# Optimization experiments

Hardware: AMD Instinct MI355X
Metric: run time of the kernel (lower is better)

The kernel has to match this reference:

```python
import jax, jax.numpy as jnp
import numpy as np

H = 64  # hidden_size hardcoded in the module


def _lstm_scan(x_pre, w_hh):
    # x_pre: [T, B, 4H] = x @ W_ih^T + b_ih + b_hh, precomputed for all steps
    # w_hh: [4H, H]. PyTorch gate order: i, f, g, o.
    B = x_pre.shape[1]
    h0 = jnp.zeros((B, H), x_pre.dtype)
    c0 = jnp.zeros((B, H), x_pre.dtype)

    def cell(carry, xp):
        h, c = carry
        gates = xp + h @ w_hh.T  # [B, 4H]
        i, f, g, o = jnp.split(gates, 4, axis=-1)
        i = jax.nn.sigmoid(i)
        f = jax.nn.sigmoid(f)
        g = jnp.tanh(g)
        o = jax.nn.sigmoid(o)
        c = f * c + i * g
        h = o * jnp.tanh(c)
        return (h, c), h

    _, hs = jax.lax.scan(cell, (h0, c0), x_pre)
    return hs  # [T, B, H]


def _bidir_layer(x, w_ih, w_hh, b_ih, b_hh):
    # x: [T, B, D]; w_ih: [2, 4H, D]; w_hh: [2, 4H, H]; b_*: [2, 4H]
    pre_f = jnp.einsum('tbd,gd->tbg', x, w_ih[0]) + b_ih[0] + b_hh[0]
    hs_f = _lstm_scan(pre_f, w_hh[0])
    xr = x[::-1]
    pre_b = jnp.einsum('tbd,gd->tbg', xr, w_ih[1]) + b_ih[1] + b_hh[1]
    hs_b = _lstm_scan(pre_b, w_hh[1])[::-1]  # re-reverse to align with time
    return jnp.concatenate([hs_f, hs_b], axis=-1)  # [T, B, 2H]


def setup_inputs() -> dict:
    key = jax.random.key(0)
    B, T, F = 1024, 512, 32
    ks = jax.random.split(key, 11)
    s = 1.0 / float(np.sqrt(H))  # PyTorch LSTM init: U(-1/sqrt(H), 1/sqrt(H))
    u = lambda k, shape: jax.random.uniform(k, shape, jnp.float32, -s, s)
    return dict(
        x=jax.random.normal(ks[0], (B, T, F), jnp.float32),
        w_ih0=u(ks[1], (2, 4 * H, F)),
        w_hh0=u(ks[2], (2, 4 * H, H)),
        b_ih0=u(ks[3], (2, 4 * H)),
        b_hh0=u(ks[4], (2, 4 * H)),
        w_ih1=u(ks[5], (2, 4 * H, 2 * H)),
        w_hh1=u(ks[6], (2, 4 * H, H)),
        b_ih1=u(ks[7], (2, 4 * H)),
        b_hh1=u(ks[8], (2, 4 * H)),
        fc_w=u(ks[9], (2, 2 * H)),
        fc_b=u(ks[10], (2,)),
    )


def reference(x, w_ih0, w_hh0, b_ih0, b_hh0, w_ih1, w_hh1, b_ih1, b_hh1, fc_w, fc_b):
    xt = jnp.transpose(x, (1, 0, 2))  # [T, B, F]
    h1 = _bidir_layer(xt, w_ih0, w_hh0, b_ih0, b_hh0)  # [T, B, 2H]
    h2 = _bidir_layer(h1, w_ih1, w_hh1, b_ih1, b_hh1)  # [T, B, 2H]
    last = h2[-1]  # out[:, -1, :] in batch_first layout -> [B, 2H]
    return last @ fc_w.T + fc_b  # [B, 2]
```

## Files before the change

kernel.cpp:

```cpp
#include <hip/hip_runtime.h>

#define TT 512
#define BB 1024
#define FF 32
#define HH 64
#define GG 256

__device__ float g_h1[(size_t)TT * BB * 2 * HH];
__device__ float g_pre0[(size_t)2 * TT * BB * GG];
__device__ float g_pre1[(size_t)TT * BB * GG];
__device__ float g_hf[(size_t)BB * HH];

__device__ __forceinline__ float fsigm(float x) {
    float e = __builtin_amdgcn_exp2f(x * -1.44269504088896f);
    return __builtin_amdgcn_rcpf(1.0f + e);
}
__device__ __forceinline__ float ftanh(float x) {
    float e = __builtin_amdgcn_exp2f(x * -2.88539008177793f);
    return 2.0f * __builtin_amdgcn_rcpf(1.0f + e) - 1.0f;
}
__device__ __forceinline__ float rlane(float v, int l) {
    return __int_as_float(__builtin_amdgcn_readlane(__float_as_int(v), l));
}

__global__ __launch_bounds__(256, 4) void pre_gemm0(
    const float* __restrict__ x,
    const float* __restrict__ w_ih,
    const float* __restrict__ b_ih,
    const float* __restrict__ b_hh)
{
    const int tid = threadIdx.x;
    const int b   = blockIdx.x >> 1;
    const int dir = blockIdx.x & 1;

    __shared__ __align__(16) float4 w4[8 * 256];
    __shared__ __align__(16) float xbuf[2][256];

    const float4* wsrc = (const float4*)(w_ih + ((size_t)dir * GG + tid) * FF);
#pragma unroll
    for (int kq = 0; kq < 8; ++kq) w4[kq * 256 + tid] = wsrc[kq];
    const float bias = b_ih[dir * GG + tid] + b_hh[dir * GG + tid];

    const float* xbase = x + (size_t)b * TT * FF;
    xbuf[0][tid] = xbase[tid];
    const size_t OS = (size_t)BB * GG;

    for (int tc = 0; tc < 64; ++tc) {
        const int cur = tc & 1;
        __syncthreads();

        float vnext = 0.f;
        if (tc + 1 < 64) vnext = xbase[(tc + 1) * 256 + tid];

        float a0 = bias, a1 = bias, a2 = bias, a3 = bias,
              a4 = bias, a5 = bias, a6 = bias, a7 = bias;
#pragma unroll
        for (int kq = 0; kq < 8; ++kq) {
            float4 wq = w4[kq * 256 + tid];
            const float4* xr = (const float4*)xbuf[cur];
            float4 q;
            q = xr[0 * 8 + kq]; a0 += q.x*wq.x + q.y*wq.y + q.z*wq.z + q.w*wq.w;
            q = xr[1 * 8 + kq]; a1 += q.x*wq.x + q.y*wq.y + q.z*wq.z + q.w*wq.w;
            q = xr[2 * 8 + kq]; a2 += q.x*wq.x + q.y*wq.y + q.z*wq.z + q.w*wq.w;
            q = xr[3 * 8 + kq]; a3 += q.x*wq.x + q.y*wq.y + q.z*wq.z + q.w*wq.w;
            q = xr[4 * 8 + kq]; a4 += q.x*wq.x + q.y*wq.y + q.z*wq.z + q.w*wq.w;
            q = xr[5 * 8 + kq]; a5 += q.x*wq.x + q.y*wq.y + q.z*wq.z + q.w*wq.w;
            q = xr[6 * 8 + kq]; a6 += q.x*wq.x + q.y*wq.y + q.z*wq.z + q.w*wq.w;
            q = xr[7 * 8 + kq]; a7 += q.x*wq.x + q.y*wq.y + q.z*wq.z + q.w*wq.w;
        }
        float* op = g_pre0 + (((size_t)dir * TT + tc * 8) * BB + b) * GG + tid;
        op[0] = a0; op[1 * OS] = a1; op[2 * OS] = a2; op[3 * OS] = a3;
        op[4 * OS] = a4; op[5 * OS] = a5; op[6 * OS] = a6; op[7 * OS] = a7;

        if (tc + 1 < 64) xbuf[1 - cur][tid] = vnext;
    }
}

#define PINQ(wq) \
    asm volatile("" : "+v"(wq.x), "+v"(wq.y), "+v"(wq.z), "+v"(wq.w))

template <int L>
__global__ __launch_bounds__(64, 1) void lstm_scan(
    const float* __restrict__ w_hh)
{
    const int l   = threadIdx.x;
    const int dir = (L == 0) ? (blockIdx.x & 1) : 0;
    const int b   = (L == 0) ? (int)(blockIdx.x >> 1) : (int)blockIdx.x;

    const float* wbase = w_hh + (size_t)dir * GG * HH;

    const float4* pi_ = (const float4*)(wbase + (size_t)(0  + l) * HH);
    const float4* pf_ = (const float4*)(wbase + (size_t)(64 + l) * HH);
    float4 wi0 = pi_[0],  wi1 = pi_[1],  wi2 = pi_[2],  wi3 = pi_[3],
           wi4 = pi_[4],  wi5 = pi_[5],  wi6 = pi_[6],  wi7 = pi_[7],
           wi8 = pi_[8],  wi9 = pi_[9],  wi10 = pi_[10], wi11 = pi_[11],
           wi12 = pi_[12], wi13 = pi_[13], wi14 = pi_[14], wi15 = pi_[15];
    float4 wf0 = pf_[0],  wf1 = pf_[1],  wf2 = pf_[2],  wf3 = pf_[3],
           wf4 = pf_[4],  wf5 = pf_[5],  wf6 = pf_[6],  wf7 = pf_[7],
           wf8 = pf_[8],  wf9 = pf_[9],  wf10 = pf_[10], wf11 = pf_[11],
           wf12 = pf_[12], wf13 = pf_[13], wf14 = pf_[14], wf15 = pf_[15];
    PINQ(wi0);  PINQ(wi1);  PINQ(wi2);  PINQ(wi3);
    PINQ(wi4);  PINQ(wi5);  PINQ(wi6);  PINQ(wi7);
    PINQ(wi8);  PINQ(wi9);  PINQ(wi10); PINQ(wi11);
    PINQ(wi12); PINQ(wi13); PINQ(wi14); PINQ(wi15);
    PINQ(wf0);  PINQ(wf1);  PINQ(wf2);  PINQ(wf3);
    PINQ(wf4);  PINQ(wf5);  PINQ(wf6);  PINQ(wf7);
    PINQ(wf8);  PINQ(wf9);  PINQ(wf10); PINQ(wf11);
    PINQ(wf12); PINQ(wf13); PINQ(wf14); PINQ(wf15);

    float4 wg[16], wo[16];
    {
        const float4* pg_ = (const float4*)(wbase + (size_t)(128 + l) * HH);
        const float4* po_ = (const float4*)(wbase + (size_t)(192 + l) * HH);
#pragma unroll
        for (int q = 0; q < 16; ++q) { wg[q] = pg_[q]; wo[q] = po_[q]; }
    }

    const float* pre = (L == 0) ? (g_pre0 + (size_t)dir * TT * BB * GG) : g_pre1;

    float c = 0.f, h = 0.f;

    const int t0 = dir ? (TT - 1) : 0;
    const int t1 = dir ? (TT - 2) : 1;
    const float* pp0 = pre + ((size_t)t0 * BB + b) * GG;
    const float* pp1 = pre + ((size_t)t1 * BB + b) * GG;
    float ci0 = pp0[l], cf0 = pp0[64 + l], cg0 = pp0[128 + l], co0 = pp0[192 + l];
    float ci1 = pp1[l], cf1 = pp1[64 + l], cg1 = pp1[128 + l], co1 = pp1[192 + l];

    for (int s = 0; s < TT; ++s) {
        const int t = dir ? (TT - 1 - s) : s;

        float ni = 0.f, nf = 0.f, ng = 0.f, no_ = 0.f;
        if (s + 2 < TT) {
            const int tn = dir ? (TT - 3 - s) : (s + 2);
            const float* np = pre + ((size_t)tn * BB + b) * GG;
            ni = np[l]; nf = np[64 + l]; ng = np[128 + l]; no_ = np[192 + l];
        }

        float ai = ci0, af = cf0, ag = cg0, ao = co0;

#define STEPQ(q) do {                                                        \
        float s0 = rlane(h, 4*q+0), s1 = rlane(h, 4*q+1),                    \
              s2 = rlane(h, 4*q+2), s3 = rlane(h, 4*q+3);                    \
        ai += s0*wi##q.x + s1*wi##q.y + s2*wi##q.z + s3*wi##q.w;             \
        af += s0*wf##q.x + s1*wf##q.y + s2*wf##q.z + s3*wf##q.w;             \
        ag += s0*wg[q].x + s1*wg[q].y + s2*wg[q].z + s3*wg[q].w;             \
        ao += s0*wo[q].x + s1*wo[q].y + s2*wo[q].z + s3*wo[q].w;             \
    } while (0)

        STEPQ(0);  STEPQ(1);  STEPQ(2);  STEPQ(3);
        STEPQ(4);  STEPQ(5);  STEPQ(6);  STEPQ(7);
        STEPQ(8);  STEPQ(9);  STEPQ(10); STEPQ(11);
        STEPQ(12); STEPQ(13); STEPQ(14); STEPQ(15);
#undef STEPQ

        const float ig = fsigm(ai);
        const float fg = fsigm(af);
        const float gg = ftanh(ag);
        const float og = fsigm(ao);
        c = fg * c + ig * gg;
        h = og * ftanh(c);

        if (L == 0) {
            g_h1[((size_t)t * BB + b) * (2 * HH) + dir * HH + l] = h;
        } else {
            if (s == TT - 1) g_hf[(size_t)b * HH + l] = h;
        }

        ci0 = ci1; cf0 = cf1; cg0 = cg1; co0 = co1;
        ci1 = ni;  cf1 = nf;  cg1 = ng;  co1 = no_;
    }
}

#define FMA4(c, s, b) do { c.x += (s)*(b).x; c.y += (s)*(b).y; \
                           c.z += (s)*(b).z; c.w += (s)*(b).w; } while (0)

__global__ __launch_bounds__(256, 2) void pre_gemm1(
    const float* __restrict__ w_ih,
    const float* __restrict__ b_ih,
    const float* __restrict__ b_hh)
{
    __shared__ __align__(16) float As[64 * 132];
    __shared__ __align__(16) float Bs[128 * 68];

    const int tid   = threadIdx.x;
    const int mbase = (int)(blockIdx.x >> 2) * 64;
    const int n0    = (int)(blockIdx.x & 3) * 64;

#pragma unroll
    for (int i = 0; i < 8; ++i) {
        const int qid = tid + 256 * i;
        const int r = qid >> 5, q = qid & 31;
        float4 v = *(const float4*)(g_h1 + (size_t)(mbase + r) * 128 + q * 4);
        *(float4*)(&As[r * 132 + q * 4]) = v;
    }
#pragma unroll
    for (int i = 0; i < 8; ++i) {
        const int qid = tid + 256 * i;
        const int r = qid >> 5, q = qid & 31;
        float4 v = *(const float4*)(w_ih + (size_t)(n0 + r) * 128 + q * 4);
        Bs[(q * 4 + 0) * 68 + r] = v.x;
        Bs[(q * 4 + 1) * 68 + r] = v.y;
        Bs[(q * 4 + 2) * 68 + r] = v.z;
        Bs[(q * 4 + 3) * 68 + r] = v.w;
    }
    __syncthreads();

    const int tx = tid & 15, ty = tid >> 4;

    float4 c0 = make_float4(0.f, 0.f, 0.f, 0.f);
    float4 c1 = c0, c2 = c0, c3 = c0;

#pragma unroll 8
    for (int kq = 0; kq < 32; ++kq) {
        const float4 a0 = *(const float4*)&As[(ty * 4 + 0) * 132 + kq * 4];
        const float4 a1 = *(const float4*)&As[(ty * 4 + 1) * 132 + kq * 4];
        const float4 a2 = *(const float4*)&As[(ty * 4 + 2) * 132 + kq * 4];
        const float4 a3 = *(const float4*)&As[(ty * 4 + 3) * 132 + kq * 4];
        const float4 b0 = *(const float4*)&Bs[(kq * 4 + 0) * 68 + tx * 4];
        const float4 b1 = *(const float4*)&Bs[(kq * 4 + 1) * 68 + tx * 4];
        const float4 b2 = *(const float4*)&Bs[(kq * 4 + 2) * 68 + tx * 4];
        const float4 b3 = *(const float4*)&Bs[(kq * 4 + 3) * 68 + tx * 4];
        FMA4(c0, a0.x, b0); FMA4(c0, a0.y, b1); FMA4(c0, a0.z, b2); FMA4(c0, a0.w, b3);
        FMA4(c1, a1.x, b0); FMA4(c1, a1.y, b1); FMA4(c1, a1.z, b2); FMA4(c1, a1.w, b3);
        FMA4(c2, a2.x, b0); FMA4(c2, a2.y, b1); FMA4(c2, a2.z, b2); FMA4(c2, a2.w, b3);
        FMA4(c3, a3.x, b0); FMA4(c3, a3.y, b1); FMA4(c3, a3.z, b2); FMA4(c3, a3.w, b3);
    }

    float4 bias4;
    bias4.x = b_ih[n0 + tx * 4 + 0] + b_hh[n0 + tx * 4 + 0];
    bias4.y = b_ih[n0 + tx * 4 + 1] + b_hh[n0 + tx * 4 + 1];
    bias4.z = b_ih[n0 + tx * 4 + 2] + b_hh[n0 + tx * 4 + 2];
    bias4.w = b_ih[n0 + tx * 4 + 3] + b_hh[n0 + tx * 4 + 3];

    FMA4(c0, 1.f, bias4); FMA4(c1, 1.f, bias4);
    FMA4(c2, 1.f, bias4); FMA4(c3, 1.f, bias4);

    float* ob = g_pre1 + (size_t)(mbase + ty * 4) * GG + n0 + tx * 4;
    *(float4*)(ob + 0 * (size_t)GG) = c0;
    *(float4*)(ob + 1 * (size_t)GG) = c1;
    *(float4*)(ob + 2 * (size_t)GG) = c2;
    *(float4*)(ob + 3 * (size_t)GG) = c3;
}

#define FMAC4(W, P0, P1, P2, P3, K) do{                                   \
    float4 v_;                                                           \
    v_ = (P0)[K]; acc0 += W.x*v_.x; acc0 += W.y*v_.y; acc0 += W.z*v_.z; acc0 += W.w*v_.w; \
    v_ = (P1)[K]; acc1 += W.x*v_.x; acc1 += W.y*v_.y; acc1 += W.z*v_.z; acc1 += W.w*v_.w; \
    v_ = (P2)[K]; acc2 += W.x*v_.x; acc2 += W.y*v_.y; acc2 += W.z*v_.z; acc2 += W.w*v_.w; \
    v_ = (P3)[K]; acc3 += W.x*v_.x; acc3 += W.y*v_.y; acc3 += W.z*v_.z; acc3 += W.w*v_.w; \
}while(0)

__global__ __launch_bounds__(256, 2) void lstm_final(
    const float* __restrict__ w_ih,
    const float* __restrict__ b_ih,
    const float* __restrict__ b_hh,
    const float* __restrict__ fc_w,
    const float* __restrict__ fc_b,
    float* __restrict__ out)
{
    const int tid = threadIdx.x;
    const int b0  = blockIdx.x * 4;

    __shared__ __align__(16) float x_lds[4][128];
    __shared__ __align__(16) float gact[4][GG];
    __shared__ __align__(16) float last[4][128];

#pragma unroll
    for (int r = 0; r < 2; ++r) {
        int idx = tid + r * 256;
        int b = idx >> 7, col = idx & 127;
        x_lds[b][col] = g_h1[((size_t)(TT - 1) * BB + (b0 + b)) * 128 + col];
    }

    const float4* p = (const float4*)(w_ih + ((size_t)GG + tid) * 128);
    float4 w0 = p[0],  w1 = p[1],  w2 = p[2],  w3 = p[3],  w4 = p[4],  w5 = p[5],
           w6 = p[6],  w7 = p[7],  w8 = p[8],  w9 = p[9],  w10 = p[10], w11 = p[11],
           w12 = p[12], w13 = p[13], w14 = p[14], w15 = p[15], w16 = p[16], w17 = p[17],
           w18 = p[18], w19 = p[19], w20 = p[20], w21 = p[21], w22 = p[22], w23 = p[23],
           w24 = p[24], w25 = p[25], w26 = p[26], w27 = p[27], w28 = p[28], w29 = p[29],
           w30 = p[30], w31 = p[31];
    const float bias = b_ih[GG + tid] + b_hh[GG + tid];
    __syncthreads();

    const float4* xb0 = (const float4*)x_lds[0];
    const float4* xb1 = (const float4*)x_lds[1];
    const float4* xb2 = (const float4*)x_lds[2];
    const float4* xb3 = (const float4*)x_lds[3];

    float acc0 = bias, acc1 = bias, acc2 = bias, acc3 = bias;
    FMAC4(w0, xb0, xb1, xb2, xb3, 0);   FMAC4(w1, xb0, xb1, xb2, xb3, 1);
    FMAC4(w2, xb0, xb1, xb2, xb3, 2);   FMAC4(w3, xb0, xb1, xb2, xb3, 3);
    FMAC4(w4, xb0, xb1, xb2, xb3, 4);   FMAC4(w5, xb0, xb1, xb2, xb3, 5);
    FMAC4(w6, xb0, xb1, xb2, xb3, 6);   FMAC4(w7, xb0, xb1, xb2, xb3, 7);
    FMAC4(w8, xb0, xb1, xb2, xb3, 8);   FMAC4(w9, xb0, xb1, xb2, xb3, 9);
    FMAC4(w10, xb0, xb1, xb2, xb3, 10); FMAC4(w11, xb0, xb1, xb2, xb3, 11);
    FMAC4(w12, xb0, xb1, xb2, xb3, 12); FMAC4(w13, xb0, xb1, xb2, xb3, 13);
    FMAC4(w14, xb0, xb1, xb2, xb3, 14); FMAC4(w15, xb0, xb1, xb2, xb3, 15);
    FMAC4(w16, xb0, xb1, xb2, xb3, 16); FMAC4(w17, xb0, xb1, xb2, xb3, 17);
    FMAC4(w18, xb0, xb1, xb2, xb3, 18); FMAC4(w19, xb0, xb1, xb2, xb3, 19);
    FMAC4(w20, xb0, xb1, xb2, xb3, 20); FMAC4(w21, xb0, xb1, xb2, xb3, 21);
    FMAC4(w22, xb0, xb1, xb2, xb3, 22); FMAC4(w23, xb0, xb1, xb2, xb3, 23);
    FMAC4(w24, xb0, xb1, xb2, xb3, 24); FMAC4(w25, xb0, xb1, xb2, xb3, 25);
    FMAC4(w26, xb0, xb1, xb2, xb3, 26); FMAC4(w27, xb0, xb1, xb2, xb3, 27);
    FMAC4(w28, xb0, xb1, xb2, xb3, 28); FMAC4(w29, xb0, xb1, xb2, xb3, 29);
    FMAC4(w30, xb0, xb1, xb2, xb3, 30); FMAC4(w31, xb0, xb1, xb2, xb3, 31);

    const bool is_g = ((tid >> 6) == 2);
    gact[0][tid] = is_g ? ftanh(acc0) : fsigm(acc0);
    gact[1][tid] = is_g ? ftanh(acc1) : fsigm(acc1);
    gact[2][tid] = is_g ? ftanh(acc2) : fsigm(acc2);
    gact[3][tid] = is_g ? ftanh(acc3) : fsigm(acc3);
    __syncthreads();

    {
        const int cb = tid >> 6, cj = tid & 63;
        float ig = gact[cb][cj];
        float gg = gact[cb][2 * HH + cj];
        float og = gact[cb][3 * HH + cj];
        float c = ig * gg;
        float h = og * ftanh(c);
        last[cb][HH + cj] = h;
        last[cb][cj] = g_hf[(size_t)(b0 + cb) * HH + cj];
    }
    __syncthreads();

    if (tid < 8) {
        int b = tid >> 1, o = tid & 1;
        float a = fc_b[o];
#pragma unroll
        for (int j = 0; j < 128; ++j) a += fc_w[o * 128 + j] * last[b][j];
        out[(size_t)(b0 + b) * 2 + o] = a;
    }
}

extern "C" void kernel_launch(void* const* d_in, const int* in_sizes, int n_in,
                              void* d_out, int out_size, void* d_ws, size_t ws_size,
                              hipStream_t stream) {
    const float* x     = (const float*)d_in[0];
    const float* w_ih0 = (const float*)d_in[1];
    const float* w_hh0 = (const float*)d_in[2];
    const float* b_ih0 = (const float*)d_in[3];
    const float* b_hh0 = (const float*)d_in[4];
    const float* w_ih1 = (const float*)d_in[5];
    const float* w_hh1 = (const float*)d_in[6];
    const float* b_ih1 = (const float*)d_in[7];
    const float* b_hh1 = (const float*)d_in[8];
    const float* fc_w  = (const float*)d_in[9];
    const float* fc_b  = (const float*)d_in[10];
    float* out = (float*)d_out;

    pre_gemm0<<<2048, 256, 0, stream>>>(x, w_ih0, b_ih0, b_hh0);
    lstm_scan<0><<<2048, 64, 0, stream>>>(w_hh0);
    pre_gemm1<<<32768, 256, 0, stream>>>(w_ih1, b_ih1, b_hh1);
    lstm_scan<1><<<1024, 64, 0, stream>>>(w_hh1);
    lstm_final<<<256, 256, 0, stream>>>(w_ih1, b_ih1, b_hh1, fc_w, fc_b, out);
}
```

Measured before the change: 2.453 ms.

## Process two batch rows per LSTM scan wavefront with g/o weights in LDS

Each single-wave block of the recurrent scan now advances two batch elements at once, reusing the register-resident i/f weights and the readlane broadcasts across both rows. The g and o weight rows move from registers into shared memory to free VGPRs for the second row's state. Grid sizes are halved to match. This doubles the useful work per weight load and gives two independent dependency chains per step for latency hiding. The cost is extra LDS reads every step and fewer blocks, which lowers parallelism across the GPU's compute units.

```diff
diff --git a/kernel.cpp b/kernel.cpp
--- a/kernel.cpp
+++ b/kernel.cpp
@@ -85,9 +85,21 @@
 {
     const int l   = threadIdx.x;
     const int dir = (L == 0) ? (blockIdx.x & 1) : 0;
-    const int b   = (L == 0) ? (int)(blockIdx.x >> 1) : (int)blockIdx.x;
+    const int b0  = ((L == 0) ? (int)(blockIdx.x >> 1) : (int)blockIdx.x) * 2;
+    const int b1  = b0 + 1;
 
     const float* wbase = w_hh + (size_t)dir * GG * HH;
+
+    __shared__ __align__(16) float4 wgo[2 * 16 * 64];
+    {
+        const float4* pg_ = (const float4*)(wbase + (size_t)(128 + l) * HH);
+        const float4* po_ = (const float4*)(wbase + (size_t)(192 + l) * HH);
+#pragma unroll
+        for (int q = 0; q < 16; ++q) {
+            wgo[q * 64 + l]        = pg_[q];
+            wgo[(16 + q) * 64 + l] = po_[q];
+        }
+    }
 
     const float4* pi_ = (const float4*)(wbase + (size_t)(0  + l) * HH);
     const float4* pf_ = (const float4*)(wbase + (size_t)(64 + l) * HH);
@@ -108,44 +120,54 @@
     PINQ(wf8);  PINQ(wf9);  PINQ(wf10); PINQ(wf11);
     PINQ(wf12); PINQ(wf13); PINQ(wf14); PINQ(wf15);
 
-    float4 wg[16], wo[16];
-    {
-        const float4* pg_ = (const float4*)(wbase + (size_t)(128 + l) * HH);
-        const float4* po_ = (const float4*)(wbase + (size_t)(192 + l) * HH);
-#pragma unroll
-        for (int q = 0; q < 16; ++q) { wg[q] = pg_[q]; wo[q] = po_[q]; }
-    }
+    __syncthreads();
 
     const float* pre = (L == 0) ? (g_pre0 + (size_t)dir * TT * BB * GG) : g_pre1;
 
-    float c = 0.f, h = 0.f;
+    float c0 = 0.f, h0 = 0.f, c1 = 0.f, h1 = 0.f;
 
     const int t0 = dir ? (TT - 1) : 0;
     const int t1 = dir ? (TT - 2) : 1;
-    const float* pp0 = pre + ((size_t)t0 * BB + b) * GG;
-    const float* pp1 = pre + ((size_t)t1 * BB + b) * GG;
-    float ci0 = pp0[l], cf0 = pp0[64 + l], cg0 = pp0[128 + l], co0 = pp0[192 + l];
-    float ci1 = pp1[l], cf1 = pp1[64 + l], cg1 = pp1[128 + l], co1 = pp1[192 + l];
+    const float* pA0 = pre + ((size_t)t0 * BB + b0) * GG;
+    const float* pA1 = pre + ((size_t)t1 * BB + b0) * GG;
+    const float* pB0 = pre + ((size_t)t0 * BB + b1) * GG;
+    const float* pB1 = pre + ((size_t)t1 * BB + b1) * GG;
+    float ci0 = pA0[l], cf0 = pA0[64+l], cg0 = pA0[128+l], co0 = pA0[192+l];
+    float ni0 = pA1[l], nf0 = pA1[64+l], ng0 = pA1[128+l], no0 = pA1[192+l];
+    float ci1 = pB0[l], cf1 = pB0[64+l], cg1 = pB0[128+l], co1 = pB0[192+l];
+    float ni1 = pB1[l], nf1 = pB1[64+l], ng1 = pB1[128+l], no1 = pB1[192+l];
 
     for (int s = 0; s < TT; ++s) {
         const int t = dir ? (TT - 1 - s) : s;
 
-        float ni = 0.f, nf = 0.f, ng = 0.f, no_ = 0.f;
+        float fi0 = 0.f, ff0 = 0.f, fg0 = 0.f, fo0 = 0.f;
+        float fi1 = 0.f, ff1 = 0.f, fg1 = 0.f, fo1 = 0.f;
         if (s + 2 < TT) {
             const int tn = dir ? (TT - 3 - s) : (s + 2);
-            const float* np = pre + ((size_t)tn * BB + b) * GG;
-            ni = np[l]; nf = np[64 + l]; ng = np[128 + l]; no_ = np[192 + l];
-        }
-
-        float ai = ci0, af = cf0, ag = cg0, ao = co0;
+            const float* npA = pre + ((size_t)tn * BB + b0) * GG;
+            const float* npB = pre + ((size_t)tn * BB + b1) * GG;
+            fi0 = npA[l]; ff0 = npA[64+l]; fg0 = npA[128+l]; fo0 = npA[192+l];
+            fi1 = npB[l]; ff1 = npB[64+l]; fg1 = npB[128+l]; fo1 = npB[192+l];
+        }
+
+        float ai0 = ci0, af0 = cf0, ag0 = cg0, ao0 = co0;
+        float ai1 = ci1, af1 = cf1, ag1 = cg1, ao1 = co1;
 
 #define STEPQ(q) do {                                                        \
-        float s0 = rlane(h, 4*q+0), s1 = rlane(h, 4*q+1),                    \
-              s2 = rlane(h, 4*q+2), s3 = rlane(h, 4*q+3);                    \
-        ai += s0*wi##q.x + s1*wi##q.y + s2*wi##q.z + s3*wi##q.w;             \
-        af += s0*wf##q.x + s1*wf##q.y + s2*wf##q.z + s3*wf##q.w;             \
-        ag += s0*wg[q].x + s1*wg[q].y + s2*wg[q].z + s3*wg[q].w;             \
-        ao += s0*wo[q].x + s1*wo[q].y + s2*wo[q].z + s3*wo[q].w;             \
+        const float4 wgq = wgo[(q) * 64 + l];                                \
+        const float4 woq = wgo[(16 + (q)) * 64 + l];                         \
+        const float s0 = rlane(h0, 4*q+0), s1 = rlane(h0, 4*q+1),            \
+                    s2 = rlane(h0, 4*q+2), s3 = rlane(h0, 4*q+3);            \
+        const float u0 = rlane(h1, 4*q+0), u1 = rlane(h1, 4*q+1),            \
+                    u2 = rlane(h1, 4*q+2), u3 = rlane(h1, 4*q+3);            \
+        ai0 += s0*wi##q.x + s1*wi##q.y + s2*wi##q.z + s3*wi##q.w;            \
+        ai1 += u0*wi##q.x + u1*wi##q.y + u2*wi##q.z + u3*wi##q.w;            \
+        af0 += s0*wf##q.x + s1*wf##q.y + s2*wf##q.z + s3*wf##q.w;            \
+        af1 += u0*wf##q.x + u1*wf##q.y + u2*wf##q.z + u3*wf##q.w;            \
+        ag0 += s0*wgq.x + s1*wgq.y + s2*wgq.z + s3*wgq.w;                    \
+        ag1 += u0*wgq.x + u1*wgq.y + u2*wgq.z + u3*wgq.w;                    \
+        ao0 += s0*woq.x + s1*woq.y + s2*woq.z + s3*woq.w;                    \
+        ao1 += u0*woq.x + u1*woq.y + u2*woq.z + u3*woq.w;                    \
     } while (0)
 
         STEPQ(0);  STEPQ(1);  STEPQ(2);  STEPQ(3);
@@ -154,21 +176,33 @@
         STEPQ(12); STEPQ(13); STEPQ(14); STEPQ(15);
 #undef STEPQ
 
-        const float ig = fsigm(ai);
-        const float fg = fsigm(af);
-        const float gg = ftanh(ag);
-        const float og = fsigm(ao);
-        c = fg * c + ig * gg;
-        h = og * ftanh(c);
+        {
+            const float ig = fsigm(ai0), fg = fsigm(af0),
+                        gg = ftanh(ag0), og = fsigm(ao0);
+            c0 = fg * c0 + ig * gg;
+            h0 = og * ftanh(c0);
+        }
+        {
+            const float ig = fsigm(ai1), fg = fsigm(af1),
+                        gg = ftanh(ag1), og = fsigm(ao1);
+            c1 = fg * c1 + ig * gg;
+            h1 = og * ftanh(c1);
+        }
 
         if (L == 0) {
-            g_h1[((size_t)t * BB + b) * (2 * HH) + dir * HH + l] = h;
+            g_h1[((size_t)t * BB + b0) * (2 * HH) + dir * HH + l] = h0;
+            g_h1[((size_t)t * BB + b1) * (2 * HH) + dir * HH + l] = h1;
         } else {
-            if (s == TT - 1) g_hf[(size_t)b * HH + l] = h;
-        }
-
-        ci0 = ci1; cf0 = cf1; cg0 = cg1; co0 = co1;
-        ci1 = ni;  cf1 = nf;  cg1 = ng;  co1 = no_;
+            if (s == TT - 1) {
+                g_hf[(size_t)b0 * HH + l] = h0;
+                g_hf[(size_t)b1 * HH + l] = h1;
+            }
+        }
+
+        ci0 = ni0; cf0 = nf0; cg0 = ng0; co0 = no0;
+        ni0 = fi0; nf0 = ff0; ng0 = fg0; no0 = fo0;
+        ci1 = ni1; cf1 = nf1; cg1 = ng1; co1 = no1;
+        ni1 = fi1; nf1 = ff1; ng1 = fg1; no1 = fo1;
     }
 }
 
@@ -351,8 +385,8 @@
     float* out = (float*)d_out;
 
     pre_gemm0<<<2048, 256, 0, stream>>>(x, w_ih0, b_ih0, b_hh0);
-    lstm_scan<0><<<2048, 64, 0, stream>>>(w_hh0);
+    lstm_scan<0><<<1024, 64, 0, stream>>>(w_hh0);
     pre_gemm1<<<32768, 256, 0, stream>>>(w_ih1, b_ih1, b_hh1);
-    lstm_scan<1><<<1024, 64, 0, stream>>>(w_hh1);
+    lstm_scan<1><<<512, 64, 0, stream>>>(w_hh1);
     lstm_final<<<256, 256, 0, stream>>>(w_ih1, b_ih1, b_hh1, fc_w, fc_b, out);
 }
```

New measurement: 3.778 ms. 54.0% more time.

## Rewrite layer-0 input projection as tiled 64x64 register-blocked GEMM

Applied to the files above, without the earlier changes.

Replaces the per-batch-row pre_gemm0 kernel, which loops over time with one output column per thread, with a 64x64 output tile GEMM that gives each thread a 4x4 register block and stages x and the transposed weights in shared memory. The grid grows to 65536 blocks, each covering 64 (t,b) rows and 64 gate columns for one direction. Output writes become float4 stores that are contiguous along the gate dimension. This is meant to improve data reuse and memory coalescing, at the cost of more blocks and reloading the weights into shared memory in every block. The x reads are strided by T*F across batch rows.

```diff
diff --git a/kernel.cpp b/kernel.cpp
--- a/kernel.cpp
+++ b/kernel.cpp
@@ -22,6 +22,9 @@
 __device__ __forceinline__ float rlane(float v, int l) {
     return __int_as_float(__builtin_amdgcn_readlane(__float_as_int(v), l));
 }
+
+#define FMA4(c, s, b) do { c.x += (s)*(b).x; c.y += (s)*(b).y; \
+                           c.z += (s)*(b).z; c.w += (s)*(b).w; } while (0)
 
 __global__ __launch_bounds__(256, 4) void pre_gemm0(
     const float* __restrict__ x,
@@ -29,51 +32,75 @@
     const float* __restrict__ b_ih,
     const float* __restrict__ b_hh)
 {
-    const int tid = threadIdx.x;
-    const int b   = blockIdx.x >> 1;
-    const int dir = blockIdx.x & 1;
-
-    __shared__ __align__(16) float4 w4[8 * 256];
-    __shared__ __align__(16) float xbuf[2][256];
-
-    const float4* wsrc = (const float4*)(w_ih + ((size_t)dir * GG + tid) * FF);
-#pragma unroll
-    for (int kq = 0; kq < 8; ++kq) w4[kq * 256 + tid] = wsrc[kq];
-    const float bias = b_ih[dir * GG + tid] + b_hh[dir * GG + tid];
-
-    const float* xbase = x + (size_t)b * TT * FF;
-    xbuf[0][tid] = xbase[tid];
-    const size_t OS = (size_t)BB * GG;
-
-    for (int tc = 0; tc < 64; ++tc) {
-        const int cur = tc & 1;
-        __syncthreads();
-
-        float vnext = 0.f;
-        if (tc + 1 < 64) vnext = xbase[(tc + 1) * 256 + tid];
-
-        float a0 = bias, a1 = bias, a2 = bias, a3 = bias,
-              a4 = bias, a5 = bias, a6 = bias, a7 = bias;
-#pragma unroll
-        for (int kq = 0; kq < 8; ++kq) {
-            float4 wq = w4[kq * 256 + tid];
-            const float4* xr = (const float4*)xbuf[cur];
-            float4 q;
-            q = xr[0 * 8 + kq]; a0 += q.x*wq.x + q.y*wq.y + q.z*wq.z + q.w*wq.w;
-            q = xr[1 * 8 + kq]; a1 += q.x*wq.x + q.y*wq.y + q.z*wq.z + q.w*wq.w;
-            q = xr[2 * 8 + kq]; a2 += q.x*wq.x + q.y*wq.y + q.z*wq.z + q.w*wq.w;
-            q = xr[3 * 8 + kq]; a3 += q.x*wq.x + q.y*wq.y + q.z*wq.z + q.w*wq.w;
-            q = xr[4 * 8 + kq]; a4 += q.x*wq.x + q.y*wq.y + q.z*wq.z + q.w*wq.w;
-            q = xr[5 * 8 + kq]; a5 += q.x*wq.x + q.y*wq.y + q.z*wq.z + q.w*wq.w;
-            q = xr[6 * 8 + kq]; a6 += q.x*wq.x + q.y*wq.y + q.z*wq.z + q.w*wq.w;
-            q = xr[7 * 8 + kq]; a7 += q.x*wq.x + q.y*wq.y + q.z*wq.z + q.w*wq.w;
-        }
-        float* op = g_pre0 + (((size_t)dir * TT + tc * 8) * BB + b) * GG + tid;
-        op[0] = a0; op[1 * OS] = a1; op[2 * OS] = a2; op[3 * OS] = a3;
-        op[4 * OS] = a4; op[5 * OS] = a5; op[6 * OS] = a6; op[7 * OS] = a7;
-
-        if (tc + 1 < 64) xbuf[1 - cur][tid] = vnext;
-    }
+    __shared__ __align__(16) float As[64 * 36];
+    __shared__ __align__(16) float Bs[32 * 68];
+
+    const int tid   = threadIdx.x;
+    const int dir   = (int)(blockIdx.x >> 15);
+    const int rem   = (int)(blockIdx.x & 32767);
+    const int mt    = rem >> 2;
+    const int n0    = (rem & 3) * 64;
+    const int mbase = mt << 6;
+    const int t     = mbase >> 10;
+    const int b0    = mbase & 1023;
+
+#pragma unroll
+    for (int i = 0; i < 2; ++i) {
+        const int qid = tid + 256 * i;
+        const int r = qid >> 3, q = qid & 7;
+        float4 v = *(const float4*)(x + ((size_t)(b0 + r) * TT + t) * FF + q * 4);
+        *(float4*)(&As[r * 36 + q * 4]) = v;
+    }
+#pragma unroll
+    for (int i = 0; i < 2; ++i) {
+        const int qid = tid + 256 * i;
+        const int r = qid >> 3, q = qid & 7;
+        float4 v = *(const float4*)(w_ih + ((size_t)dir * GG + n0 + r) * FF + q * 4);
+        Bs[(q * 4 + 0) * 68 + r] = v.x;
+        Bs[(q * 4 + 1) * 68 + r] = v.y;
+        Bs[(q * 4 + 2) * 68 + r] = v.z;
+        Bs[(q * 4 + 3) * 68 + r] = v.w;
+    }
+    __syncthreads();
+
+    const int tx = tid & 15, ty = tid >> 4;
+
+    float4 c0 = make_float4(0.f, 0.f, 0.f, 0.f);
+    float4 c1 = c0, c2 = c0, c3 = c0;
+
+#pragma unroll
+    for (int kq = 0; kq < 8; ++kq) {
+        const float4 a0 = *(const float4*)&As[(ty * 4 + 0) * 36 + kq * 4];
+        const float4 a1 = *(const float4*)&As[(ty * 4 + 1) * 36 + kq * 4];
+        const float4 a2 = *(const float4*)&As[(ty * 4 + 2) * 36 + kq * 4];
+        const float4 a3 = *(const float4*)&As[(ty * 4 + 3) * 36 + kq * 4];
+        const float4 b0_ = *(const float4*)&Bs[(kq * 4 + 0) * 68 + tx * 4];
+        const float4 b1_ = *(const float4*)&Bs[(kq * 4 + 1) * 68 + tx * 4];
+        const float4 b2_ = *(const float4*)&Bs[(kq * 4 + 2) * 68 + tx * 4];
+        const float4 b3_ = *(const float4*)&Bs[(kq * 4 + 3) * 68 + tx * 4];
+        FMA4(c0, a0.x, b0_); FMA4(c0, a0.y, b1_); FMA4(c0, a0.z, b2_); FMA4(c0, a0.w, b3_);
+        FMA4(c1, a1.x, b0_); FMA4(c1, a1.y, b1_); FMA4(c1, a1.z, b2_); FMA4(c1, a1.w, b3_);
+        FMA4(c2, a2.x, b0_); FMA4(c2, a2.y, b1_); FMA4(c2, a2.z, b2_); FMA4(c2, a2.w, b3_);
+        FMA4(c3, a3.x, b0_); FMA4(c3, a3.y, b1_); FMA4(c3, a3.z, b2_); FMA4(c3, a3.w, b3_);
+    }
+
+    float4 bias4;
+    {
+        const int g = dir * GG + n0 + tx * 4;
+        bias4.x = b_ih[g + 0] + b_hh[g + 0];
+        bias4.y = b_ih[g + 1] + b_hh[g + 1];
+        bias4.z = b_ih[g + 2] + b_hh[g + 2];
+        bias4.w = b_ih[g + 3] + b_hh[g + 3];
+    }
+    FMA4(c0, 1.f, bias4); FMA4(c1, 1.f, bias4);
+    FMA4(c2, 1.f, bias4); FMA4(c3, 1.f, bias4);
+
+    float* ob = g_pre0 +
+        (((size_t)dir * TT + t) * BB + (b0 + ty * 4)) * GG + n0 + tx * 4;
+    *(float4*)(ob + 0 * (size_t)GG) = c0;
+    *(float4*)(ob + 1 * (size_t)GG) = c1;
+    *(float4*)(ob + 2 * (size_t)GG) = c2;
+    *(float4*)(ob + 3 * (size_t)GG) = c3;
 }
 
 #define PINQ(wq) \
@@ -172,9 +199,6 @@
     }
 }
 
-#define FMA4(c, s, b) do { c.x += (s)*(b).x; c.y += (s)*(b).y; \
-                           c.z += (s)*(b).z; c.w += (s)*(b).w; } while (0)
-
 __global__ __launch_bounds__(256, 2) void pre_gemm1(
     const float* __restrict__ w_ih,
     const float* __restrict__ b_ih,
@@ -350,7 +374,7 @@
     const float* fc_b  = (const float*)d_in[10];
     float* out = (float*)d_out;
 
-    pre_gemm0<<<2048, 256, 0, stream>>>(x, w_ih0, b_ih0, b_hh0);
+    pre_gemm0<<<65536, 256, 0, stream>>>(x, w_ih0, b_ih0, b_hh0);
     lstm_scan<0><<<2048, 64, 0, stream>>>(w_hh0);
     pre_gemm1<<<32768, 256, 0, stream>>>(w_ih1, b_ih1, b_hh1);
     lstm_scan<1><<<1024, 64, 0, stream>>>(w_hh1);
```

After: 2.570 ms. 1.05x slower.
